# Optimization experiments

Measured on AMD Instinct MI355X. Metric: run time of the kernel, lower is better.

## Reference

```python
import jax, jax.numpy as jnp
import numpy as np

B, T, D = 32, 512, 512


def setup_inputs() -> dict:
    key = jax.random.key(0)
    kx, kd = jax.random.split(key)
    x = jax.random.normal(kx, (B, T, D), dtype=jnp.float32)
    dur = jax.random.randint(kd, (B, T), 0, 8, dtype=jnp.int64)
    return {"x": x, "dur": dur}


def reference(x, dur):
    # x: [B, T, D] encoder features; dur: [B, T] integer durations (frames per token)
    dur = jnp.maximum(dur, 0)                      # duration[duration < 0] = 0
    tot = jnp.cumsum(dur, axis=1)                  # [B, T] cumulative end positions
    max_duration = int(jnp.max(tot[:, -1]))        # padded expanded length (eager concretization)
    frames = jnp.arange(max_duration)              # [M]
    # frame t maps to first token j with cumsum > t (zero-duration tokens are skipped);
    # frames past a row's total map past T and are clipped to the last token (matches
    # the original's trailing fill with j = T-1).
    idx = jax.vmap(lambda row: jnp.searchsorted(row, frames, side='right'))(tot)  # [B, M]
    idx = jnp.clip(idx, 0, x.shape[1] - 1)
    return jnp.take_along_axis(x, idx[:, :, None], axis=1)  # [B, M, D]
```

## Files before the change

### kernel.cpp

```cpp
#include <hip/hip_runtime.h>


#define B_BATCH 32
#define T_TOK   512
#define D_DIM   512
#define DQ      (D_DIM / 4)
#define TPB     4
#define TAILB   32

__global__ __launch_bounds__(T_TOK)
void lr_scan(const int* __restrict__ dur,
             int* __restrict__ start, int* __restrict__ total) {
    __shared__ int s[T_TOK];
    const int b = blockIdx.x;
    const int t = threadIdx.x;

    int d = dur[b * T_TOK + t];
    if (d < 0) d = 0;

    s[t] = d;
    __syncthreads();
    #pragma unroll
    for (int off = 1; off < T_TOK; off <<= 1) {
        int v = (t >= off) ? s[t - off] : 0;
        __syncthreads();
        s[t] += v;
        __syncthreads();
    }
    const int tot = s[t];
    start[b * T_TOK + t] = tot - d;
    if (t == T_TOK - 1) total[b] = tot;
}

__global__ __launch_bounds__(2 * T_TOK > 512 ? 512 : 512)
void lr_expand(const float4* __restrict__ x,
               const int* __restrict__ dur,
               const int* __restrict__ start,
               const int* __restrict__ total,
               float4* __restrict__ out, int M) {
    const int b   = blockIdx.y;
    const int q   = threadIdx.x & (DQ - 1);
    const int sub = threadIdx.x >> 7;

    if (blockIdx.x < T_TOK / TPB) {
        const int t = blockIdx.x * TPB + sub;
        int d = dur[b * T_TOK + t];
        if (d <= 0) return;
        const float4 v = x[((size_t)b * T_TOK + t) * DQ + q];
        const int st = start[b * T_TOK + t];
        float4* o = out + ((size_t)b * M + st) * DQ + q;
        for (int k = 0; k < d; ++k) o[k * DQ] = v;
    } else {
        const int tot = total[b];
        if (tot >= M) return;
        const float4 v = x[((size_t)b * T_TOK + (T_TOK - 1)) * DQ + q];
        const int j = blockIdx.x - T_TOK / TPB;
        for (int r = tot + j * TPB + sub; r < M; r += TAILB * TPB)
            out[((size_t)b * M + r) * DQ + q] = v;
    }
}

extern "C" void kernel_launch(void* const* d_in, const int* in_sizes, int n_in,
                              void* d_out, int out_size, void* d_ws, size_t ws_size,
                              hipStream_t stream) {
    const float* x = (const float*)d_in[0];
    const int* dur = (const int*)d_in[1];
    float* out     = (float*)d_out;

    const int M = out_size / (B_BATCH * D_DIM);

    int* start = (int*)d_ws;
    int* total = start + B_BATCH * T_TOK;

    lr_scan<<<B_BATCH, T_TOK, 0, stream>>>(dur, start, total);

    dim3 grid(T_TOK / TPB + TAILB, B_BATCH);
    lr_expand<<<grid, TPB * DQ, 0, stream>>>((const float4*)x, dur, start, total,
                                             (float4*)out, M);
}
```

Measured before the change: 153.7 us.

## Fuse duration scan into expand kernel and use nontemporal stores

```diff
diff --git a/kernel.cpp b/kernel.cpp
--- a/kernel.cpp
+++ b/kernel.cpp
@@ -1,62 +1,68 @@
 #include <hip/hip_runtime.h>
 
+
+typedef float f32x4 __attribute__((ext_vector_type(4)));
 
 #define B_BATCH 32
 #define T_TOK   512
 #define D_DIM   512
 #define DQ      (D_DIM / 4)
 #define TPB     4
+#define MAINB   (T_TOK / TPB)
 #define TAILB   32
 
-__global__ __launch_bounds__(T_TOK)
-void lr_scan(const int* __restrict__ dur,
-             int* __restrict__ start, int* __restrict__ total) {
-    __shared__ int s[T_TOK];
-    const int b = blockIdx.x;
-    const int t = threadIdx.x;
+__global__ __launch_bounds__(TPB * DQ)
+void lr_fused(const f32x4* __restrict__ x,
+              const int* __restrict__ dur,
+              f32x4* __restrict__ out, int M) {
+    __shared__ int s[T_TOK + 1];
+    const int b = blockIdx.y;
 
-    int d = dur[b * T_TOK + t];
-    if (d < 0) d = 0;
+    if (threadIdx.x < 64) {
+        const int l = threadIdx.x;
+        const int4* drow = (const int4*)(dur + b * T_TOK);
+        int4 a0 = drow[l * 2];
+        int4 a1 = drow[l * 2 + 1];
+        int v[8] = {a0.x, a0.y, a0.z, a0.w, a1.x, a1.y, a1.z, a1.w};
+        int p[8], run = 0;
+        #pragma unroll
+        for (int k = 0; k < 8; ++k) {
+            int d = v[k] > 0 ? v[k] : 0;
+            p[k] = run;
+            run += d;
+        }
+        int inc = run;
+        #pragma unroll
+        for (int off = 1; off < 64; off <<= 1) {
+            int u = __shfl_up(inc, off);
+            if (l >= off) inc += u;
+        }
+        const int base = inc - run;
+        #pragma unroll
+        for (int k = 0; k < 8; ++k) s[l * 8 + k] = base + p[k];
+        if (l == 63) s[T_TOK] = inc;
+    }
+    __syncthreads();
 
-    s[t] = d;
-    __syncthreads();
-    #pragma unroll
-    for (int off = 1; off < T_TOK; off <<= 1) {
-        int v = (t >= off) ? s[t - off] : 0;
-        __syncthreads();
-        s[t] += v;
-        __syncthreads();
-    }
-    const int tot = s[t];
-    start[b * T_TOK + t] = tot - d;
-    if (t == T_TOK - 1) total[b] = tot;
-}
-
-__global__ __launch_bounds__(2 * T_TOK > 512 ? 512 : 512)
-void lr_expand(const float4* __restrict__ x,
-               const int* __restrict__ dur,
-               const int* __restrict__ start,
-               const int* __restrict__ total,
-               float4* __restrict__ out, int M) {
-    const int b   = blockIdx.y;
     const int q   = threadIdx.x & (DQ - 1);
     const int sub = threadIdx.x >> 7;
 
-    if (blockIdx.x < T_TOK / TPB) {
-        const int t = blockIdx.x * TPB + sub;
-        int d = dur[b * T_TOK + t];
-        if (d <= 0) return;
-        const float4 v = x[((size_t)b * T_TOK + t) * DQ + q];
-        const int st = start[b * T_TOK + t];
-        float4* o = out + ((size_t)b * M + st) * DQ + q;
-        for (int k = 0; k < d; ++k) o[k * DQ] = v;
+    if (blockIdx.x < MAINB) {
+        const int t  = blockIdx.x * TPB + sub;
+        const int st = s[t];
+        const int en = s[t + 1];
+        if (en <= st) return;
+        const f32x4 v = x[((size_t)b * T_TOK + t) * DQ + q];
+        f32x4* o = out + ((size_t)b * M + st) * DQ + q;
+        for (int r = st; r < en; ++r, o += DQ)
+            __builtin_nontemporal_store(v, o);
     } else {
-        const int tot = total[b];
+        const int tot = s[T_TOK];
         if (tot >= M) return;
-        const float4 v = x[((size_t)b * T_TOK + (T_TOK - 1)) * DQ + q];
-        const int j = blockIdx.x - T_TOK / TPB;
+        const f32x4 v = x[((size_t)b * T_TOK + (T_TOK - 1)) * DQ + q];
+        const int j = blockIdx.x - MAINB;
         for (int r = tot + j * TPB + sub; r < M; r += TAILB * TPB)
-            out[((size_t)b * M + r) * DQ + q] = v;
+            __builtin_nontemporal_store(v, out + ((size_t)b * M + r) * DQ + q);
     }
 }
 
@@ -69,12 +75,7 @@
 
     const int M = out_size / (B_BATCH * D_DIM);
 
-    int* start = (int*)d_ws;
-    int* total = start + B_BATCH * T_TOK;
-
-    lr_scan<<<B_BATCH, T_TOK, 0, stream>>>(dur, start, total);
-
-    dim3 grid(T_TOK / TPB + TAILB, B_BATCH);
-    lr_expand<<<grid, TPB * DQ, 0, stream>>>((const float4*)x, dur, start, total,
-                                             (float4*)out, M);
+    dim3 grid(MAINB + TAILB, B_BATCH);
+    lr_fused<<<grid, TPB * DQ, 0, stream>>>((const f32x4*)x, dur,
+                                            (f32x4*)out, M);
 }
```

After: 154.2 us. No clear change (+0.3%).
